# Optimization experiments

Measured on AMD Instinct MI355X. Metric: run time of the kernel, lower is better.

## Reference

```python
import jax, jax.numpy as jnp
import numpy as np

B, L, H, VOCAB, MAXLEN = 128, 256, 512, 32000, 256
DEPTH = 8  # L == 2**DEPTH complete binary trees

# Level offsets for internal nodes stored level-major (level 1 = just above leaves)
_OFF = np.zeros(DEPTH + 1, dtype=np.int64)
_s = 0
for _k in range(1, DEPTH + 1):
    _OFF[_k] = _s
    _s += L >> _k

# Post-order permutation of internal nodes (matches the iterative left-first
# traversal order in which the torch code appends hs)
def _post(k, j, acc):
    if k == 0:
        return
    _post(k - 1, 2 * j, acc)
    _post(k - 1, 2 * j + 1, acc)
    acc.append(int(_OFF[k]) + j)

_acc = []
_post(DEPTH, 0, _acc)
POST = np.asarray(_acc, dtype=np.int64)  # (L-1,)


def setup_inputs() -> dict:
    key = jax.random.key(0)
    ks = jax.random.split(key, 18)
    s = 1.0 / np.sqrt(H)
    d = {
        'word_idx': jax.random.randint(ks[0], (B, L), 0, VOCAB),
        'emb': jax.random.normal(ks[1], (VOCAB, H), jnp.float32) * s,
    }
    names = ['U_i_l', 'U_i_r', 'U_fl_l', 'U_fl_r', 'U_fr_l', 'U_fr_r',
             'U_o_l', 'U_o_r', 'U_c_l', 'U_c_r']
    for i, n in enumerate(names):
        d[n] = jax.random.normal(ks[2 + i], (H, H), jnp.float32) * s
    for i, n in enumerate(['b_i', 'b_fl', 'b_fr', 'b_o', 'b_c']):
        d[n] = jax.random.normal(ks[12 + i], (H,), jnp.float32) * 0.1
    return d


def reference(word_idx, emb, U_i_l, U_i_r, b_i, U_fl_l, U_fl_r, b_fl,
              U_fr_l, U_fr_r, b_fr, U_o_l, U_o_r, b_o, U_c_l, U_c_r, b_c):
    # Fuse the 5 gate projections per side into one GEMM: (5H, H)
    Wl = jnp.concatenate([U_i_l, U_fl_l, U_fr_l, U_o_l, U_c_l], axis=0)
    Wr = jnp.concatenate([U_i_r, U_fl_r, U_fr_r, U_o_r, U_c_r], axis=0)
    b = jnp.concatenate([b_i, b_fl, b_fr, b_o, b_c], axis=0)

    def combine(hl, hr, cl, cr):
        # hl/hr: (B, n, H); torch does U @ h with h (H,1) -> h @ U.T batched
        z = jnp.einsum('bnh,gh->bng', hl, Wl) + jnp.einsum('bnh,gh->bng', hr, Wr) + b
        i, fl, fr, o, c = jnp.split(z, 5, axis=-1)
        c_phr = jax.nn.sigmoid(i) * jnp.tanh(c) \
            + jax.nn.sigmoid(fl) * cl + jax.nn.sigmoid(fr) * cr
        h_phr = jax.nn.sigmoid(o) * jnp.tanh(c_phr)
        return h_phr, c_phr

    # Leaves: h = embedding row, c = 0.5 (torch: ones - 0.5)
    h = emb[word_idx]                      # (B, L, H)
    c = jnp.full((B, L, H), 0.5, emb.dtype)

    internal_hs = []
    for _ in range(DEPTH):  # level-synchronous bottom-up combine
        h, c = combine(h[:, 0::2], h[:, 1::2], c[:, 0::2], c[:, 1::2])
        internal_hs.append(h)

    H_int = jnp.concatenate(internal_hs, axis=1)  # (B, L-1, H), level-major
    post = jnp.asarray(POST)
    # torch bug faithfully reproduced: hs[0] is prepended, then all hs appended
    out = jnp.concatenate([H_int[:, post[:1]], H_int[:, post]], axis=1)  # (B, MAXLEN, H)

    forest_h = jnp.swapaxes(h, 0, 1)  # (1, B, H)
    forest_c = jnp.swapaxes(c, 0, 1)  # (1, B, H)
    return out, (forest_h, forest_c)
```

## Files before the change

kernel.cpp:

```cpp
#include <hip/hip_runtime.h>

#define NB 128
#define NL 256
#define NH 512
#define NMAX 256

typedef __attribute__((ext_vector_type(8))) short s8v;
typedef __attribute__((ext_vector_type(4))) float f4v;

struct Params {
  const int* widx;
  const float* bias[5];
  const unsigned short* wbf;
  const unsigned short* embbf;
  const unsigned short* hcprev;
  unsigned short* hcout;
  unsigned short* part;
  float* out;
  float* fh;
  float* fc;
};

struct PrepParams {
  const float* u[10];
  const float* emb;
  unsigned short* wdst;
  unsigned short* edst;
};

__device__ __forceinline__ float bf2f(unsigned short u) {
  union { unsigned int i; float f; } v;
  v.i = ((unsigned int)u) << 16;
  return v.f;
}
__device__ __forceinline__ unsigned short f2bf(float f) {
  union { float f; unsigned int i; } v;
  v.f = f;
  unsigned int x = v.i;
  x += 0x7fffu + ((x >> 16) & 1u);
  return (unsigned short)(x >> 16);
}
__device__ __forceinline__ s8v pack8(f4v a, f4v b) {
  s8v r;
  r[0] = (short)f2bf(a[0]); r[1] = (short)f2bf(a[1]);
  r[2] = (short)f2bf(a[2]); r[3] = (short)f2bf(a[3]);
  r[4] = (short)f2bf(b[0]); r[5] = (short)f2bf(b[1]);
  r[6] = (short)f2bf(b[2]); r[7] = (short)f2bf(b[3]);
  return r;
}
__device__ __forceinline__ float sigf(float x) {
  return 1.f / (1.f + __expf(-x));
}
__device__ __forceinline__ void glds16(const void* g, void* l) {
  __builtin_amdgcn_global_load_lds(
      (const __attribute__((address_space(1))) unsigned int*)g,
      (__attribute__((address_space(3))) unsigned int*)l, 16, 0, 0);
}

__global__ __launch_bounds__(256) void prep_cvt(PrepParams pp) {
  int gid = blockIdx.x * 256 + threadIdx.x;
  const float* s;
  unsigned short* d;
  if (gid < 327680) {
    int mat = gid >> 15, off = (gid & 32767) * 8;
    s = pp.u[mat] + off;
    d = pp.wdst + (size_t)mat * NH * NH + off;
  } else {
    size_t off = (size_t)(gid - 327680) * 8;
    s = pp.emb + off;
    d = pp.edst + off;
  }
  f4v x0 = *(const f4v*)s;
  f4v x1 = *(const f4v*)(s + 4);
  *(s8v*)d = pack8(x0, x1);
}


template<int LEVEL, int BM, int KS, int TILES>
__global__ __launch_bounds__(BM * 2, 2)
void lstm_level(Params p) {
  constexpr int NK = NL >> LEVEL;
  constexpr int LOGNK = 8 - LEVEL;
  constexpr int NKP = NL >> (LEVEL - 1);
  constexpr int M = NB * NK;
  constexpr int W = BM / 32;
  constexpr int ASUB = BM * 64;
  constexpr int BUFSZ = ASUB + 20480;
  constexpr int NT = 32 / KS;
  __shared__ __align__(16) unsigned char lds[2 * BUFSZ];

  const int tid = threadIdx.x;
  const int wid = tid >> 6;
  const int lane = tid & 63;
  const int lhi = lane >> 4, llo = lane & 15;
  const int mh = (BM == 256) ? (wid & 1) : 0;
  const int q  = (BM == 256) ? (wid >> 1) : wid;
  const int ht = blockIdx.y;
  const int ks = (KS > 1) ? blockIdx.z : 0;
  const int t0 = ks * NT;

  const unsigned short* abase = (LEVEL == 1) ? p.embbf : p.hcprev;

  int aOffL[2], aOffR[2];
  auto computeA = [&](int bm) {
#pragma unroll
    for (int ii = 0; ii < 2; ++ii) {
      int gi = ii * W + wid;
      int ar = gi * 16 + (lane >> 2);
      int ck = (lane & 3) ^ ((ar >> 1) & 3);
      int am = bm * BM + ar; if (am > M - 1) am = M - 1;
      int b = am >> LOGNK, j = am & (NK - 1);
      if constexpr (LEVEL == 1) {
        aOffL[ii] = p.widx[b * NL + 2 * j] * NH + ck * 8;
        aOffR[ii] = p.widx[b * NL + 2 * j + 1] * NH + ck * 8;
      } else {
        int base = (b * NKP + 2 * j) * (2 * NH);
        aOffL[ii] = base + ck * 8;
        aOffR[ii] = base + 2 * NH + ck * 8;
      }
    }
  };

  constexpr int BI = (20 + W - 1) / W;
  int bOff[BI];
#pragma unroll
  for (int ii = 0; ii < BI; ++ii) {
    int gi = ii * W + wid;
    if (gi < 20) {
      int r = gi * 16 + (lane >> 2);
      int gg = gi >> 2;
      int ck = (lane & 3) ^ ((r >> 1) & 3);
      bOff[ii] = ((2 * gg) * NH + (ht * 64 + (r & 63))) * NH + ck * 8;
    } else bOff[ii] = 0;
  }

  auto do_stage = [&](int buf, int tt) {
    unsigned char* base = lds + buf * BUFSZ;
    const int kw = (tt & 15) * 32;
    const int* ao = (tt < 16) ? aOffL : aOffR;
#pragma unroll
    for (int ii = 0; ii < 2; ++ii)
      glds16(abase + ao[ii] + kw, base + (ii * W + wid) * 1024);
    const size_t wsel = (size_t)(tt >> 4) * NH * NH;
#pragma unroll
    for (int ii = 0; ii < BI; ++ii) {
      int gi = ii * W + wid;
      if (gi < 20)
        glds16(p.wbf + wsel + bOff[ii] + kw, base + ASUB + gi * 1024);
    }
  };

  int aoff[8], boff[5];
#pragma unroll
  for (int fm = 0; fm < 8; ++fm) {
    int r = mh * 128 + fm * 16 + llo;
    aoff[fm] = r * 64 + ((lhi ^ ((r >> 1) & 3)) << 4);
  }
#pragma unroll
  for (int g = 0; g < 5; ++g) {
    int r = g * 64 + q * 16 + llo;
    boff[g] = ASUB + r * 64 + ((lhi ^ ((r >> 1) & 3)) << 4);
  }

  f4v acc[8][5];

  auto compute = [&](int buf) {
    const unsigned char* base = lds + buf * BUFSZ;
    s8v af[8], bv[5];
#pragma unroll
    for (int fm = 0; fm < 8; ++fm) af[fm] = *(const s8v*)(base + aoff[fm]);
#pragma unroll
    for (int g = 0; g < 5; ++g)  bv[g] = *(const s8v*)(base + boff[g]);
    __builtin_amdgcn_s_setprio(1);
#pragma unroll
    for (int fm = 0; fm < 8; ++fm)
#pragma unroll
      for (int g = 0; g < 5; ++g)
        acc[fm][g] = __builtin_amdgcn_mfma_f32_16x16x32_bf16(
            af[fm], bv[g], acc[fm][g], 0, 0, 0);
    __builtin_amdgcn_s_setprio(0);
  };

  const int hdl = q * 16 + llo;
  float bb[5];
#pragma unroll
  for (int g = 0; g < 5; ++g) bb[g] = p.bias[g][ht * 64 + hdl];

  int bmCur = blockIdx.x * TILES;
  computeA(bmCur);
  do_stage(0, t0);

#pragma unroll
  for (int it = 0; it < TILES; ++it) {
#pragma unroll
    for (int fm = 0; fm < 8; ++fm)
#pragma unroll
      for (int g = 0; g < 5; ++g)
        acc[fm][g] = (f4v){0.f, 0.f, 0.f, 0.f};
    __syncthreads();
    for (int t = 0; t < NT; ++t) {
      const int cur = t & 1;
      if (t + 1 < NT) do_stage(cur ^ 1, t0 + t + 1);
      compute(cur);
      if (t + 1 < NT) __syncthreads();
    }
    const int bmOut = bmCur;
    if (it + 1 < TILES) {
      bmCur = blockIdx.x * TILES + it + 1;
      computeA(bmCur);
      do_stage(0, t0);
    }

    if constexpr (KS > 1) {
#pragma unroll
      for (int fm = 0; fm < 8; ++fm) {
#pragma unroll
        for (int jj = 0; jj < 4; ++jj) {
          int m = bmOut * BM + mh * 128 + fm * 16 + lhi * 4 + jj;
          size_t base = (((size_t)(ks * M + m) * 8 + ht) * 5) * 64;
#pragma unroll
          for (int g = 0; g < 5; ++g)
            p.part[base + g * 64 + hdl] = f2bf(acc[fm][g][jj]);
        }
      }
    } else {
      const int hd = ht * 64 + hdl;
#pragma unroll
      for (int fm = 0; fm < 8; ++fm) {
#pragma unroll
        for (int jj = 0; jj < 4; ++jj) {
          int m = bmOut * BM + mh * 128 + fm * 16 + lhi * 4 + jj;
          if (m < M) {
            int b = m >> LOGNK, j = m & (NK - 1);
            float zi  = acc[fm][0][jj] + bb[0];
            float zfl = acc[fm][1][jj] + bb[1];
            float zfr = acc[fm][2][jj] + bb[2];
            float zo  = acc[fm][3][jj] + bb[3];
            float zc  = acc[fm][4][jj] + bb[4];
            float cl = 0.5f, cr = 0.5f;
            if constexpr (LEVEL > 1) {
              const unsigned short* cb =
                  p.hcprev + ((size_t)b * NKP + 2 * j) * (2 * NH) + NH;
              cl = bf2f(cb[hd]);
              cr = bf2f(cb[2 * NH + hd]);
            }
            float cnew = sigf(zi) * tanhf(zc) + sigf(zfl) * cl + sigf(zfr) * cr;
            float hnew = sigf(zo) * tanhf(cnew);
            unsigned short* orow = p.hcout + ((size_t)b * NK + j) * (2 * NH);
            orow[hd] = f2bf(hnew);
            orow[NH + hd] = f2bf(cnew);
            int colout = (((j + 1) << LEVEL) - 2 - __popc(j)) + 1;
            p.out[((size_t)b * NMAX + colout) * NH + hd] = hnew;
            if (LEVEL == 1 && j == 0) p.out[(size_t)b * NMAX * NH + hd] = hnew;
            if constexpr (LEVEL == 8) { p.fh[b * NH + hd] = hnew; p.fc[b * NH + hd] = cnew; }
          }
        }
      }
    }
  }
}

template<int LEVEL, int KS>
__global__ __launch_bounds__(256)
void lstm_combine(Params p) {
  constexpr int NK = NL >> LEVEL;
  constexpr int LOGNK = 8 - LEVEL;
  constexpr int NKP = NL >> (LEVEL - 1);
  constexpr int M = NB * NK;
  int t = blockIdx.x * 256 + threadIdx.x;
  int m = t >> 9, hd = t & 511;
  int ht = hd >> 6, hdl = hd & 63;
  int b = m >> LOGNK, j = m & (NK - 1);

  float z[5];
#pragma unroll
  for (int g = 0; g < 5; ++g) z[g] = p.bias[g][hd];
  for (int ks = 0; ks < KS; ++ks) {
    size_t base = (((size_t)(ks * M + m) * 8 + ht) * 5) * 64;
#pragma unroll
    for (int g = 0; g < 5; ++g) z[g] += bf2f(p.part[base + g * 64 + hdl]);
  }
  const unsigned short* cb = p.hcprev + ((size_t)b * NKP + 2 * j) * (2 * NH) + NH;
  float cl = bf2f(cb[hd]);
  float cr = bf2f(cb[2 * NH + hd]);
  float cnew = sigf(z[0]) * tanhf(z[4]) + sigf(z[1]) * cl + sigf(z[2]) * cr;
  float hnew = sigf(z[3]) * tanhf(cnew);
  unsigned short* orow = p.hcout + ((size_t)b * NK + j) * (2 * NH);
  orow[hd] = f2bf(hnew);
  orow[NH + hd] = f2bf(cnew);
  int colout = (((j + 1) << LEVEL) - 2 - __popc(j)) + 1;
  p.out[((size_t)b * NMAX + colout) * NH + hd] = hnew;
  if constexpr (LEVEL == 8) { p.fh[b * NH + hd] = hnew; p.fc[b * NH + hd] = cnew; }
}

extern "C" void kernel_launch(void* const* d_in, const int* in_sizes, int n_in,
                              void* d_out, int out_size, void* d_ws, size_t ws_size,
                              hipStream_t stream) {
  unsigned short* wbf = (unsigned short*)d_ws;
  unsigned short* R1  = wbf + (size_t)10 * NH * NH;
  unsigned short* R2  = R1 + 16777216;

  PrepParams pp;
  for (int i = 0; i < 10; ++i) pp.u[i] = (const float*)d_in[2 + i];
  pp.emb  = (const float*)d_in[1];
  pp.wdst = wbf;
  pp.edst = R1;

  Params p;
  p.widx = (const int*)d_in[0];
  for (int g = 0; g < 5; ++g) p.bias[g] = (const float*)d_in[12 + g];
  p.wbf   = wbf;
  p.embbf = R1;
  p.part  = nullptr;
  p.out   = (float*)d_out;
  p.fh    = p.out + (size_t)NB * NMAX * NH;
  p.fc    = p.fh + NB * NH;

  prep_cvt<<<dim3(9280), dim3(256), 0, stream>>>(pp);

  unsigned short* lvlout[9];
  for (int k = 1; k <= 8; ++k) lvlout[k] = (k & 1) ? R2 : R1;

  p.hcprev = nullptr;     p.hcout = lvlout[1];
  lstm_level<1, 256, 1, 2><<<dim3(32, 8), dim3(512), 0, stream>>>(p);
  p.hcprev = lvlout[1];   p.hcout = lvlout[2];
  lstm_level<2, 128, 1, 1><<<dim3(64, 8), dim3(256), 0, stream>>>(p);
  p.hcprev = lvlout[2];   p.hcout = lvlout[3];
  lstm_level<3, 128, 1, 1><<<dim3(32, 8), dim3(256), 0, stream>>>(p);

  p.hcprev = lvlout[3];   p.hcout = lvlout[4];
  p.part   = lvlout[3] + 6 * 1024 * 1024;
  lstm_level<4, 128, 2, 1><<<dim3(16, 8, 2), dim3(256), 0, stream>>>(p);
  lstm_combine<4, 2><<<dim3(4096), dim3(256), 0, stream>>>(p);

  p.hcprev = lvlout[4];   p.hcout = lvlout[5];
  p.part   = lvlout[4] + 4 * 1024 * 1024;
  lstm_level<5, 128, 4, 1><<<dim3(8, 8, 4), dim3(256), 0, stream>>>(p);
  lstm_combine<5, 4><<<dim3(2048), dim3(256), 0, stream>>>(p);

  p.hcprev = lvlout[5];   p.hcout = lvlout[6];
  p.part   = lvlout[5] + 4 * 1024 * 1024;
  lstm_level<6, 128, 4, 1><<<dim3(4, 8, 4), dim3(256), 0, stream>>>(p);
  lstm_combine<6, 4><<<dim3(1024), dim3(256), 0, stream>>>(p);

  p.hcprev = lvlout[6];   p.hcout = lvlout[7];
  p.part   = lvlout[6] + 4 * 1024 * 1024;
  lstm_level<7, 128, 8, 1><<<dim3(2, 8, 8), dim3(256), 0, stream>>>(p);
  lstm_combine<7, 8><<<dim3(512), dim3(256), 0, stream>>>(p);

  p.hcprev = lvlout[7];   p.hcout = lvlout[8];
  p.part   = lvlout[7] + 4 * 1024 * 1024;
  lstm_level<8, 128, 8, 1><<<dim3(1, 8, 8), dim3(256), 0, stream>>>(p);
  lstm_combine<8, 8><<<dim3(256), dim3(256), 0, stream>>>(p);
}
```

Before: 302.8 us.

## Deepen level-1 GEMM pipeline to four LDS buffers with vmcnt-based raw barriers

The level-1 kernel gets a PIPE variant. It fuses both output tiles into one continuous 64-stage loop and prefetches two stages ahead into a ring of four LDS buffers. Each stage synchronises with explicit `s_waitcnt vmcnt` counts, set per wave to match its own load count, plus a raw `s_barrier` instead of `__syncthreads`. The aim is to hide global-to-LDS latency and avoid draining the pipeline between tiles. In exchange, LDS use roughly doubles to about 144KB per block, which likely cuts residency to one block per CU. The hand-tuned wait counts are also fragile.

```diff
diff --git a/kernel.cpp b/kernel.cpp
--- a/kernel.cpp
+++ b/kernel.cpp
@@ -56,6 +56,13 @@
       (const __attribute__((address_space(1))) unsigned int*)g,
       (__attribute__((address_space(3))) unsigned int*)l, 16, 0, 0);
 }
+__device__ __forceinline__ void barrier_raw() {
+  __builtin_amdgcn_sched_barrier(0);
+  __builtin_amdgcn_s_barrier();
+  __builtin_amdgcn_sched_barrier(0);
+}
+#define WAITV(N) do { asm volatile("s_waitcnt vmcnt(" #N ")" ::: "memory"); \
+                      __builtin_amdgcn_sched_barrier(0); } while (0)
 
 __global__ __launch_bounds__(256) void prep_cvt(PrepParams pp) {
   int gid = blockIdx.x * 256 + threadIdx.x;
@@ -76,7 +83,7 @@
 }
 
 
-template<int LEVEL, int BM, int KS, int TILES>
+template<int LEVEL, int BM, int KS, int TILES, int PIPE>
 __global__ __launch_bounds__(BM * 2, 2)
 void lstm_level(Params p) {
   constexpr int NK = NL >> LEVEL;
@@ -87,7 +94,8 @@
   constexpr int ASUB = BM * 64;
   constexpr int BUFSZ = ASUB + 20480;
   constexpr int NT = 32 / KS;
-  __shared__ __align__(16) unsigned char lds[2 * BUFSZ];
+  constexpr int NBUF = PIPE ? 4 : 2;
+  __shared__ __align__(16) unsigned char lds[NBUF * BUFSZ];
 
   const int tid = threadIdx.x;
   const int wid = tid >> 6;
@@ -134,13 +142,8 @@
     } else bOff[ii] = 0;
   }
 
-  auto do_stage = [&](int buf, int tt) {
-    unsigned char* base = lds + buf * BUFSZ;
+  auto stageB = [&](unsigned char* base, int tt) {
     const int kw = (tt & 15) * 32;
-    const int* ao = (tt < 16) ? aOffL : aOffR;
-#pragma unroll
-    for (int ii = 0; ii < 2; ++ii)
-      glds16(abase + ao[ii] + kw, base + (ii * W + wid) * 1024);
     const size_t wsel = (size_t)(tt >> 4) * NH * NH;
 #pragma unroll
     for (int ii = 0; ii < BI; ++ii) {
@@ -149,6 +152,17 @@
         glds16(p.wbf + wsel + bOff[ii] + kw, base + ASUB + gi * 1024);
     }
   };
+  auto stageA2 = [&](unsigned char* base, int o0, int o1, int kw) {
+    glds16(abase + o0 + kw, base + (0 * W + wid) * 1024);
+    glds16(abase + o1 + kw, base + (1 * W + wid) * 1024);
+  };
+  auto do_stage = [&](int buf, int tt) {
+    unsigned char* base = lds + buf * BUFSZ;
+    const int kw = (tt & 15) * 32;
+    const int* ao = (tt < 16) ? aOffL : aOffR;
+    stageA2(base, ao[0], ao[1], kw);
+    stageB(base, tt);
+  };
 
   int aoff[8], boff[5];
 #pragma unroll
@@ -186,31 +200,7 @@
 #pragma unroll
   for (int g = 0; g < 5; ++g) bb[g] = p.bias[g][ht * 64 + hdl];
 
-  int bmCur = blockIdx.x * TILES;
-  computeA(bmCur);
-  do_stage(0, t0);
-
-#pragma unroll
-  for (int it = 0; it < TILES; ++it) {
-#pragma unroll
-    for (int fm = 0; fm < 8; ++fm)
-#pragma unroll
-      for (int g = 0; g < 5; ++g)
-        acc[fm][g] = (f4v){0.f, 0.f, 0.f, 0.f};
-    __syncthreads();
-    for (int t = 0; t < NT; ++t) {
-      const int cur = t & 1;
-      if (t + 1 < NT) do_stage(cur ^ 1, t0 + t + 1);
-      compute(cur);
-      if (t + 1 < NT) __syncthreads();
-    }
-    const int bmOut = bmCur;
-    if (it + 1 < TILES) {
-      bmCur = blockIdx.x * TILES + it + 1;
-      computeA(bmCur);
-      do_stage(0, t0);
-    }
-
+  auto epilogue = [&](int bmOut) {
     if constexpr (KS > 1) {
 #pragma unroll
       for (int fm = 0; fm < 8; ++fm) {
@@ -257,6 +247,76 @@
         }
       }
     }
+  };
+
+  if constexpr (PIPE) {
+    computeA(blockIdx.x * TILES);
+    int aL0_0 = aOffL[0], aL0_1 = aOffL[1], aR0_0 = aOffR[0], aR0_1 = aOffR[1];
+    computeA(blockIdx.x * TILES + 1);
+    int aL1_0 = aOffL[0], aL1_1 = aOffL[1], aR1_0 = aOffR[0], aR1_1 = aOffR[1];
+
+    auto stageP = [&](int buf, int s) {
+      unsigned char* base = lds + buf * BUFSZ;
+      const bool sec = s >= 32;
+      const int tt = s & 31;
+      const int kw = (tt & 15) * 32;
+      int o0, o1;
+      if (tt < 16) { o0 = sec ? aL1_0 : aL0_0; o1 = sec ? aL1_1 : aL0_1; }
+      else         { o0 = sec ? aR1_0 : aR0_0; o1 = sec ? aR1_1 : aR0_1; }
+      stageA2(base, o0, o1, kw);
+      stageB(base, tt);
+    };
+
+#pragma unroll
+    for (int fm = 0; fm < 8; ++fm)
+#pragma unroll
+      for (int g = 0; g < 5; ++g)
+        acc[fm][g] = (f4v){0.f, 0.f, 0.f, 0.f};
+
+    stageP(0, 0);
+    stageP(1, 1);
+    for (int s = 0; s < 64; ++s) {
+      if (s + 2 < 64) stageP((s + 2) & 3, s + 2);
+      if (s < 62)      { if (wid < 4) { WAITV(10); } else { WAITV(8); } }
+      else if (s == 62){ if (wid < 4) { WAITV(5);  } else { WAITV(4); } }
+      else             { WAITV(0); }
+      barrier_raw();
+      compute(s & 3);
+      if ((s & 31) == 31) {
+        epilogue(blockIdx.x * TILES + (s >> 5));
+#pragma unroll
+        for (int fm = 0; fm < 8; ++fm)
+#pragma unroll
+          for (int g = 0; g < 5; ++g)
+            acc[fm][g] = (f4v){0.f, 0.f, 0.f, 0.f};
+      }
+    }
+  } else {
+    int bmCur = blockIdx.x * TILES;
+    computeA(bmCur);
+    do_stage(0, t0);
+#pragma unroll
+    for (int it = 0; it < TILES; ++it) {
+#pragma unroll
+      for (int fm = 0; fm < 8; ++fm)
+#pragma unroll
+        for (int g = 0; g < 5; ++g)
+          acc[fm][g] = (f4v){0.f, 0.f, 0.f, 0.f};
+      __syncthreads();
+      for (int t = 0; t < NT; ++t) {
+        const int cur = t & 1;
+        if (t + 1 < NT) do_stage(cur ^ 1, t0 + t + 1);
+        compute(cur);
+        if (t + 1 < NT) __syncthreads();
+      }
+      const int bmOut = bmCur;
+      if (it + 1 < TILES) {
+        bmCur = blockIdx.x * TILES + it + 1;
+        computeA(bmCur);
+        do_stage(0, t0);
+      }
+      epilogue(bmOut);
+    }
   }
 }
 
@@ -322,34 +382,34 @@
   for (int k = 1; k <= 8; ++k) lvlout[k] = (k & 1) ? R2 : R1;
 
   p.hcprev = nullptr;     p.hcout = lvlout[1];
-  lstm_level<1, 256, 1, 2><<<dim3(32, 8), dim3(512), 0, stream>>>(p);
+  lstm_level<1, 256, 1, 2, 1><<<dim3(32, 8), dim3(512), 0, stream>>>(p);
   p.hcprev = lvlout[1];   p.hcout = lvlout[2];
-  lstm_level<2, 128, 1, 1><<<dim3(64, 8), dim3(256), 0, stream>>>(p);
+  lstm_level<2, 128, 1, 1, 0><<<dim3(64, 8), dim3(256), 0, stream>>>(p);
   p.hcprev = lvlout[2];   p.hcout = lvlout[3];
-  lstm_level<3, 128, 1, 1><<<dim3(32, 8), dim3(256), 0, stream>>>(p);
+  lstm_level<3, 128, 1, 1, 0><<<dim3(32, 8), dim3(256), 0, stream>>>(p);
 
   p.hcprev = lvlout[3];   p.hcout = lvlout[4];
   p.part   = lvlout[3] + 6 * 1024 * 1024;
-  lstm_level<4, 128, 2, 1><<<dim3(16, 8, 2), dim3(256), 0, stream>>>(p);
+  lstm_level<4, 128, 2, 1, 0><<<dim3(16, 8, 2), dim3(256), 0, stream>>>(p);
   lstm_combine<4, 2><<<dim3(4096), dim3(256), 0, stream>>>(p);
 
   p.hcprev = lvlout[4];   p.hcout = lvlout[5];
   p.part   = lvlout[4] + 4 * 1024 * 1024;
-  lstm_level<5, 128, 4, 1><<<dim3(8, 8, 4), dim3(256), 0, stream>>>(p);
+  lstm_level<5, 128, 4, 1, 0><<<dim3(8, 8, 4), dim3(256), 0, stream>>>(p);
   lstm_combine<5, 4><<<dim3(2048), dim3(256), 0, stream>>>(p);
 
   p.hcprev = lvlout[5];   p.hcout = lvlout[6];
   p.part   = lvlout[5] + 4 * 1024 * 1024;
-  lstm_level<6, 128, 4, 1><<<dim3(4, 8, 4), dim3(256), 0, stream>>>(p);
+  lstm_level<6, 128, 4, 1, 0><<<dim3(4, 8, 4), dim3(256), 0, stream>>>(p);
   lstm_combine<6, 4><<<dim3(1024), dim3(256), 0, stream>>>(p);
 
   p.hcprev = lvlout[6];   p.hcout = lvlout[7];
   p.part   = lvlout[6] + 4 * 1024 * 1024;
-  lstm_level<7, 128, 8, 1><<<dim3(2, 8, 8), dim3(256), 0, stream>>>(p);
+  lstm_level<7, 128, 8, 1, 0><<<dim3(2, 8, 8), dim3(256), 0, stream>>>(p);
   lstm_combine<7, 8><<<dim3(512), dim3(256), 0, stream>>>(p);
 
   p.hcprev = lvlout[7];   p.hcout = lvlout[8];
   p.part   = lvlout[7] + 4 * 1024 * 1024;
-  lstm_level<8, 128, 8, 1><<<dim3(1, 8, 8), dim3(256), 0, stream>>>(p);
+  lstm_level<8, 128, 8, 1, 0><<<dim3(1, 8, 8), dim3(256), 0, stream>>>(p);
   lstm_combine<8, 8><<<dim3(256), dim3(256), 0, stream>>>(p);
 }
```

After: 506.6 us. 1.67x slower.
